# Performance work log

Measured on AMD Instinct MI355X. Metric: run time of the kernel, lower is better.

The kernel has to match this reference:

```python
import jax, jax.numpy as jnp
import numpy as np

HIDDEN = 2048
N_HEADS = 32
N_KV_HEADS = 8
HEAD_DIM = HIDDEN // N_HEADS  # 64
KV_DIM = N_KV_HEADS * HEAD_DIM  # 512


def setup_inputs() -> dict:
    key = jax.random.key(0)
    ks = jax.random.split(key, 9)
    s = 1.0 / np.sqrt(HIDDEN)
    x = jax.random.normal(ks[0], (2, 2048, HIDDEN), dtype=jnp.float32)
    wq = jax.random.uniform(ks[1], (HIDDEN, HIDDEN), jnp.float32, -s, s)
    bq = jax.random.uniform(ks[2], (HIDDEN,), jnp.float32, -s, s)
    wk = jax.random.uniform(ks[3], (KV_DIM, HIDDEN), jnp.float32, -s, s)
    bk = jax.random.uniform(ks[4], (KV_DIM,), jnp.float32, -s, s)
    wv = jax.random.uniform(ks[5], (KV_DIM, HIDDEN), jnp.float32, -s, s)
    bv = jax.random.uniform(ks[6], (KV_DIM,), jnp.float32, -s, s)
    wo = jax.random.uniform(ks[7], (HIDDEN, HIDDEN), jnp.float32, -s, s)
    bo = jax.random.uniform(ks[8], (HIDDEN,), jnp.float32, -s, s)
    return {"x": x, "wq": wq, "bq": bq, "wk": wk, "bk": bk,
            "wv": wv, "bv": bv, "wo": wo, "bo": bo}


def reference(x, wq, bq, wk, bk, wv, bv, wo, bo):
    B, S, _ = x.shape
    group = N_HEADS // N_KV_HEADS  # 4
    # projections (torch Linear: x @ W.T + b)
    q = (x @ wq.T + bq).reshape(B, S, N_HEADS, HEAD_DIM).transpose(0, 2, 1, 3)      # [B,H,S,D]
    k = (x @ wk.T + bk).reshape(B, S, N_KV_HEADS, HEAD_DIM).transpose(0, 2, 1, 3)   # [B,Hk,S,D]
    v = (x @ wv.T + bv).reshape(B, S, N_KV_HEADS, HEAD_DIM).transpose(0, 2, 1, 3)
    # repeat_interleave KV heads to match query heads
    k = jnp.repeat(k, group, axis=1)  # [B,H,S,D]
    v = jnp.repeat(v, group, axis=1)
    scale = 1.0 / np.sqrt(HEAD_DIM).astype(np.float32)
    attn = jnp.einsum('bhqd,bhkd->bhqk', q, k) * scale  # [B,H,S,S]
    score = jax.nn.softmax(attn, axis=-1)
    out = jnp.einsum('bhqk,bhkd->bhqd', score, v)       # [B,H,S,D]
    out = out.transpose(0, 2, 1, 3).reshape(B, S, HIDDEN)
    return out @ wo.T + bo
```

## Files before the change

### kernel.cpp

```cpp
#include <hip/hip_runtime.h>

typedef __attribute__((ext_vector_type(8))) short bf16x8;
typedef __attribute__((ext_vector_type(4))) float f32x4;
typedef __attribute__((ext_vector_type(16))) float f32x16;
typedef __attribute__((ext_vector_type(2))) float f32x2;

__device__ __forceinline__ short f2b(float f) {
  union { unsigned u; float f; } c;
  c.f = f;
  unsigned r = (c.u + 0x7FFFu + ((c.u >> 16) & 1u)) >> 16;
  return (short)r;
}

__device__ __forceinline__ int cvt_pk_bf16(float lo, float hi) {
  int r;
  asm("v_cvt_pk_bf16_f32 %0, %1, %2" : "=v"(r) : "v"(lo), "v"(hi));
  return r;
}

__device__ __forceinline__ void plswap(int& a, int& b) {
  asm volatile("v_permlane32_swap_b32 %0, %1" : "+v"(a), "+v"(b));
}

__device__ __forceinline__ f32x2 pk_add(f32x2 a, f32x2 b) {
  f32x2 d;
  asm("v_pk_add_f32 %0, %1, %2" : "=v"(d) : "v"(a), "v"(b));
  return d;
}

__device__ __forceinline__ unsigned permb(unsigned s0, unsigned s1, unsigned sel) {
  unsigned d;
  asm("v_perm_b32 %0, %1, %2, %3" : "=v"(d) : "v"(s0), "v"(s1), "s"(sel));
  return d;
}

__device__ __forceinline__ void async16(const void* g, void* l) {
  __builtin_amdgcn_global_load_lds(
      (const __attribute__((address_space(1))) unsigned*)g,
      (__attribute__((address_space(3))) unsigned*)l, 16, 0, 0);
}

__global__ __launch_bounds__(256)
void conv_all(const float* __restrict__ x,  const float* __restrict__ wq,
              const float* __restrict__ wk, const float* __restrict__ wv,
              const float* __restrict__ wo, short* __restrict__ dst) {
  const size_t M = 1048576;
  size_t i = ((size_t)blockIdx.x * 256 + threadIdx.x) * 4;
  const float* src; size_t off;
  if (i < 8 * M)       { src = x;  off = 0; }
  else if (i < 12 * M) { src = wq; off = 8 * M; }
  else if (i < 13 * M) { src = wk; off = 12 * M; }
  else if (i < 14 * M) { src = wv; off = 13 * M; }
  else                 { src = wo; off = 14 * M; }
  float4 v = *(const float4*)(src + (i - off));
  short4 o;
  o.x = f2b(v.x); o.y = f2b(v.y); o.z = f2b(v.z); o.w = f2b(v.w);
  *(short4*)(dst + i) = o;
}

template <bool F32OUT>
__global__ __launch_bounds__(256)
void gemm_bt_bias(const short* __restrict__ A, const short* __restrict__ Bw,
                  const float* __restrict__ bias, void* __restrict__ Cv,
                  int M, int N, int K) {
  __shared__ short lsA[128 * 32];
  __shared__ short lsB[128 * 32];
  const int tid  = threadIdx.x;
  const int wave = tid >> 6, lane = tid & 63;
  const int quad = lane >> 4, lrow = lane & 15;
  const int m0 = blockIdx.y * 128, n0 = blockIdx.x * 128;
  const int wm = (wave >> 1) * 64, wn = (wave & 1) * 64;

  f32x4 zero = {0.f, 0.f, 0.f, 0.f};
  f32x4 acc[4][4];
#pragma unroll
  for (int i = 0; i < 4; i++)
#pragma unroll
    for (int j = 0; j < 4; j++) acc[i][j] = zero;

  const int r0 = tid >> 2, c0 = (tid & 3) * 8;
  const short* Ab  = A  + (size_t)(m0 + r0) * K + c0;
  const short* Ab2 = A  + (size_t)(m0 + r0 + 64) * K + c0;
  const short* Bb  = Bw + (size_t)(n0 + r0) * K + c0;
  const short* Bb2 = Bw + (size_t)(n0 + r0 + 64) * K + c0;

  for (int k0 = 0; k0 < K; k0 += 32) {
    async16(Ab  + k0, lsA + tid * 8);
    async16(Ab2 + k0, lsA + (tid + 256) * 8);
    async16(Bb  + k0, lsB + tid * 8);
    async16(Bb2 + k0, lsB + (tid + 256) * 8);
    __syncthreads();

    bf16x8 af[4], bfr[4];
#pragma unroll
    for (int i = 0; i < 4; i++)
      af[i] = *(const bf16x8*)(lsA + (wm + i * 16 + lrow) * 32 + quad * 8);
#pragma unroll
    for (int j = 0; j < 4; j++)
      bfr[j] = *(const bf16x8*)(lsB + (wn + j * 16 + lrow) * 32 + quad * 8);
#pragma unroll
    for (int i = 0; i < 4; i++)
#pragma unroll
      for (int j = 0; j < 4; j++)
        acc[i][j] = __builtin_amdgcn_mfma_f32_16x16x32_bf16(af[i], bfr[j], acc[i][j], 0, 0, 0);
    __syncthreads();
  }

#pragma unroll
  for (int j = 0; j < 4; j++) {
    const int col = n0 + wn + j * 16 + lrow;
    const float bv = bias[col];
#pragma unroll
    for (int i = 0; i < 4; i++) {
      const int rowb = m0 + wm + i * 16 + quad * 4;
#pragma unroll
      for (int r = 0; r < 4; r++) {
        const float val = acc[i][j][r] + bv;
        if (F32OUT)
          ((float*)Cv)[(size_t)(rowb + r) * N + col] = val;
        else
          ((short*)Cv)[(size_t)(rowb + r) * N + col] = f2b(val);
      }
    }
  }
}

__global__ __launch_bounds__(256)
void gemm_qkv(const short* __restrict__ A, const short* __restrict__ Bw,
              const float* __restrict__ bq, const float* __restrict__ bk,
              const float* __restrict__ bv,
              short* __restrict__ Qo, short* __restrict__ Ko, short* __restrict__ Vo) {
  const int K = 2048;
  __shared__ short lsA[128 * 32];
  __shared__ short lsB[128 * 32];
  const int tid  = threadIdx.x;
  const int wave = tid >> 6, lane = tid & 63;
  const int quad = lane >> 4, lrow = lane & 15;
  const int m0 = blockIdx.y * 128, n0 = blockIdx.x * 128;
  const int wm = (wave >> 1) * 64, wn = (wave & 1) * 64;

  f32x4 zero = {0.f, 0.f, 0.f, 0.f};
  f32x4 acc[4][4];
#pragma unroll
  for (int i = 0; i < 4; i++)
#pragma unroll
    for (int j = 0; j < 4; j++) acc[i][j] = zero;

  const int r0 = tid >> 2, c0 = (tid & 3) * 8;
  const short* Ab  = A  + (size_t)(m0 + r0) * K + c0;
  const short* Ab2 = A  + (size_t)(m0 + r0 + 64) * K + c0;
  const short* Bb  = Bw + (size_t)(n0 + r0) * K + c0;
  const short* Bb2 = Bw + (size_t)(n0 + r0 + 64) * K + c0;

  for (int k0 = 0; k0 < K; k0 += 32) {
    async16(Ab  + k0, lsA + tid * 8);
    async16(Ab2 + k0, lsA + (tid + 256) * 8);
    async16(Bb  + k0, lsB + tid * 8);
    async16(Bb2 + k0, lsB + (tid + 256) * 8);
    __syncthreads();

    bf16x8 af[4], bfr[4];
#pragma unroll
    for (int i = 0; i < 4; i++)
      af[i] = *(const bf16x8*)(lsA + (wm + i * 16 + lrow) * 32 + quad * 8);
#pragma unroll
    for (int j = 0; j < 4; j++)
      bfr[j] = *(const bf16x8*)(lsB + (wn + j * 16 + lrow) * 32 + quad * 8);
#pragma unroll
    for (int i = 0; i < 4; i++)
#pragma unroll
      for (int j = 0; j < 4; j++)
        acc[i][j] = __builtin_amdgcn_mfma_f32_16x16x32_bf16(af[i], bfr[j], acc[i][j], 0, 0, 0);
    __syncthreads();
  }

  short* base; int stride, coff; const float* bias;
  if (n0 < 2048)      { base = Qo; stride = 2048; bias = bq; coff = 0; }
  else if (n0 < 2560) { base = Ko; stride = 512;  bias = bk; coff = 2048; }
  else                { base = Vo; stride = 512;  bias = bv; coff = 2560; }
  const float qs = (n0 < 2048) ? 0.18033688011112043f : 1.0f;

#pragma unroll
  for (int j = 0; j < 4; j++) {
    const int lc = n0 + wn + j * 16 + lrow - coff;
    const float bvv = bias[lc];
#pragma unroll
    for (int i = 0; i < 4; i++) {
      const int rowb = m0 + wm + i * 16 + quad * 4;
#pragma unroll
      for (int r = 0; r < 4; r++)
        base[(size_t)(rowb + r) * stride + lc] = f2b((acc[i][j][r] + bvv) * qs);
    }
  }
}

#define S_LEN 2048
#define HID   2048
#define KVD   512
#define ST    72

__global__ __launch_bounds__(256)
void gqa_flash(const short* __restrict__ Q, const short* __restrict__ Kb,
               const short* __restrict__ Vb, short* __restrict__ O) {
  __shared__ __align__(16) short lsK[64 * ST];
  __shared__ __align__(16) short lsVt[64 * ST];
  __shared__ float lsum[4][32];

  const int tid  = threadIdx.x;
  const int wave = tid >> 6, lane = tid & 63;
  const int l31  = lane & 31, hl = lane >> 5;

  const int d  = blockIdx.x + (blockIdx.y << 6);
  const int by = ((d & 7) << 1) | (d >> 9);
  const int qb = (d >> 3) & 63;
  const int b = by >> 3, kvh = by & 7;
  const int h = kvh * 4 + wave;
  const int q0 = qb * 32;

  const short* Qrow = Q + (size_t)(b * S_LEN + q0 + l31) * HID + h * 64 + hl * 8;
  bf16x8 qf[4];
#pragma unroll
  for (int f = 0; f < 4; f++) qf[f] = *(const bf16x8*)(Qrow + f * 16);

  f32x16 o0, o1;
#pragma unroll
  for (int i = 0; i < 16; i++) { o0[i] = 0.f; o1[i] = 0.f; }
  float lloc = 0.f;

  const short* Kp = Kb + (size_t)b * S_LEN * KVD + kvh * 64;
  const short* Vp = Vb + (size_t)b * S_LEN * KVD + kvh * 64;

  const int keyA = tid >> 3, chK = (tid & 7) * 8;
  const int kpV = tid & 31, dcV = (tid >> 5) * 8;

  bf16x8 kf0 = *(const bf16x8*)(Kp + (size_t)keyA * KVD + chK);
  bf16x8 kf1 = *(const bf16x8*)(Kp + (size_t)(keyA + 32) * KVD + chK);
  bf16x8 vf0 = *(const bf16x8*)(Vp + (size_t)(2 * kpV) * KVD + dcV);
  bf16x8 vf1 = *(const bf16x8*)(Vp + (size_t)(2 * kpV + 1) * KVD + dcV);

  for (int k0 = 0; k0 < S_LEN; k0 += 64) {
    *(bf16x8*)(lsK + keyA * ST + chK) = kf0;
    *(bf16x8*)(lsK + (keyA + 32) * ST + chK) = kf1;
    {
      const unsigned* u0 = (const unsigned*)&vf0;
      const unsigned* u1 = (const unsigned*)&vf1;
#pragma unroll
      for (int jw = 0; jw < 4; jw++) {
        unsigned lo = permb(u1[jw], u0[jw], 0x05040100u);
        unsigned hi = permb(u1[jw], u0[jw], 0x07060302u);
        *(unsigned*)(lsVt + (dcV + 2 * jw)     * ST + 2 * kpV) = lo;
        *(unsigned*)(lsVt + (dcV + 2 * jw + 1) * ST + 2 * kpV) = hi;
      }
    }
    __syncthreads();

    const int kn = (k0 + 64) & (S_LEN - 1);
    kf0 = *(const bf16x8*)(Kp + (size_t)(kn + keyA) * KVD + chK);
    kf1 = *(const bf16x8*)(Kp + (size_t)(kn + keyA + 32) * KVD + chK);
    vf0 = *(const bf16x8*)(Vp + (size_t)(kn + 2 * kpV) * KVD + dcV);
    vf1 = *(const bf16x8*)(Vp + (size_t)(kn + 2 * kpV + 1) * KVD + dcV);

    f32x16 s0, s1;
#pragma unroll
    for (int i = 0; i < 16; i++) { s0[i] = 0.f; s1[i] = 0.f; }
    __builtin_amdgcn_s_setprio(1);
#pragma unroll
    for (int f = 0; f < 4; f++) {
      bf16x8 ka = *(const bf16x8*)(lsK + l31 * ST + f * 16 + hl * 8);
      bf16x8 kb = *(const bf16x8*)(lsK + (32 + l31) * ST + f * 16 + hl * 8);
      s0 = __builtin_amdgcn_mfma_f32_32x32x16_bf16(ka, qf[f], s0, 0, 0, 0);
      s1 = __builtin_amdgcn_mfma_f32_32x32x16_bf16(kb, qf[f], s1, 0, 0, 0);
    }
    __builtin_amdgcn_s_setprio(0);

#pragma unroll
    for (int i = 0; i < 16; i++) {
      s0[i] = __builtin_amdgcn_exp2f(s0[i]);
      s1[i] = __builtin_amdgcn_exp2f(s1[i]);
    }
    {
      const f32x2* p0 = (const f32x2*)&s0;
      const f32x2* p1 = (const f32x2*)&s1;
      f32x2 t0 = pk_add(p0[0], p1[0]);
      f32x2 t1 = pk_add(p0[1], p1[1]);
      f32x2 t2 = pk_add(p0[2], p1[2]);
      f32x2 t3 = pk_add(p0[3], p1[3]);
      f32x2 t4 = pk_add(p0[4], p1[4]);
      f32x2 t5 = pk_add(p0[5], p1[5]);
      f32x2 t6 = pk_add(p0[6], p1[6]);
      f32x2 t7 = pk_add(p0[7], p1[7]);
      t0 = pk_add(t0, t4); t1 = pk_add(t1, t5);
      t2 = pk_add(t2, t6); t3 = pk_add(t3, t7);
      t0 = pk_add(t0, t2); t1 = pk_add(t1, t3);
      t0 = pk_add(t0, t1);
      lloc += t0.x + t0.y;
    }
    int P2[2][8];
#pragma unroll
    for (int qq = 0; qq < 8; qq++) {
      P2[0][qq] = cvt_pk_bf16(s0[2 * qq], s0[2 * qq + 1]);
      P2[1][qq] = cvt_pk_bf16(s1[2 * qq], s1[2 * qq + 1]);
    }

    __builtin_amdgcn_s_setprio(1);
#pragma unroll
    for (int t = 0; t < 4; t++) {
      const int j = t >> 1, b0 = (t & 1) * 4;
      int w0 = P2[j][b0 + 0], w2 = P2[j][b0 + 2];
      int w1 = P2[j][b0 + 1], w3 = P2[j][b0 + 3];
      plswap(w0, w2);
      plswap(w1, w3);
      union { unsigned u[4]; bf16x8 v; } pa;
      pa.u[0] = (unsigned)w0; pa.u[1] = (unsigned)w1;
      pa.u[2] = (unsigned)w2; pa.u[3] = (unsigned)w3;
      bf16x8 bv0 = *(const bf16x8*)(lsVt + l31 * ST + t * 16 + hl * 8);
      bf16x8 bv1 = *(const bf16x8*)(lsVt + (32 + l31) * ST + t * 16 + hl * 8);
      o0 = __builtin_amdgcn_mfma_f32_32x32x16_bf16(pa.v, bv0, o0, 0, 0, 0);
      o1 = __builtin_amdgcn_mfma_f32_32x32x16_bf16(pa.v, bv1, o1, 0, 0, 0);
    }
    __builtin_amdgcn_s_setprio(0);
    __syncthreads();
  }

  const float lfull = lloc + __shfl(lloc, lane ^ 32);
  if (lane < 32) lsum[wave][lane] = lfull;
#pragma unroll
  for (int r = 0; r < 16; r++) {
    const int qrow = (r & 3) + 8 * (r >> 2) + 4 * hl;
    const float rl = 1.0f / lsum[wave][qrow];
    short* op = O + (size_t)(b * S_LEN + q0 + qrow) * HID + h * 64 + l31;
    op[0]  = f2b(o0[r] * rl);
    op[32] = f2b(o1[r] * rl);
  }
}

extern "C" void kernel_launch(void* const* d_in, const int* in_sizes, int n_in,
                              void* d_out, int out_size, void* d_ws, size_t ws_size,
                              hipStream_t stream) {
  const float* x  = (const float*)d_in[0];
  const float* wq = (const float*)d_in[1];
  const float* bq = (const float*)d_in[2];
  const float* wk = (const float*)d_in[3];
  const float* bk = (const float*)d_in[4];
  const float* wv = (const float*)d_in[5];
  const float* bv = (const float*)d_in[6];
  const float* wo = (const float*)d_in[7];
  const float* bo = (const float*)d_in[8];
  float* out = (float*)d_out;

  short* xb  = (short*)d_ws;
  short* wqb = xb  + (size_t)4096 * 2048;
  short* wkb = wqb + (size_t)2048 * 2048;
  short* wvb = wkb + (size_t)512 * 2048;
  short* wob = wvb + (size_t)512 * 2048;
  short* Qb  = wob + (size_t)2048 * 2048;
  short* Kb  = Qb  + (size_t)4096 * 2048;
  short* Vb  = Kb  + (size_t)4096 * 512;
  short* AO  = Vb  + (size_t)4096 * 512;

  dim3 blk(256);
  conv_all<<<18 * 1048576 / 1024, blk, 0, stream>>>(x, wq, wk, wv, wo, xb);

  gemm_qkv<<<dim3(3072 / 128, 4096 / 128), blk, 0, stream>>>(xb, wqb, bq, bk, bv, Qb, Kb, Vb);
  gqa_flash<<<dim3(2048 / 32, 16), blk, 0, stream>>>(Qb, Kb, Vb, AO);
  gemm_bt_bias<true><<<dim3(2048 / 128, 4096 / 128), blk, 0, stream>>>(AO, wob, bo, out, 4096, 2048, 2048);
}
```

Before: 320.1 us.

## Widen GEMM k-tile with XOR-swizzled LDS and software-pipeline flash attention

Both GEMM kernels now stage 64-wide k-slices in LDS instead of 32-wide ones. Rows are stored with an XOR swizzle on 16-byte chunks, which halves the number of barrier pairs per K sweep and is meant to avoid LDS bank conflicts on the fragment reads. The attention kernel gets double-buffered K and V tiles: the P·V product of the previous tile is issued after the QK and softmax of the current tile, so MFMA work can overlap the exp/pack stage. The asm volatile on permlane swap is relaxed so the compiler can schedule it. The cost is twice the LDS per block and more live registers for the carried P fragments, which may lower occupancy.

```diff
diff --git a/kernel.cpp b/kernel.cpp
--- a/kernel.cpp
+++ b/kernel.cpp
@@ -19,7 +19,7 @@
 }
 
 __device__ __forceinline__ void plswap(int& a, int& b) {
-  asm volatile("v_permlane32_swap_b32 %0, %1" : "+v"(a), "+v"(b));
+  asm("v_permlane32_swap_b32 %0, %1" : "+v"(a), "+v"(b));
 }
 
 __device__ __forceinline__ f32x2 pk_add(f32x2 a, f32x2 b) {
@@ -63,8 +63,8 @@
 void gemm_bt_bias(const short* __restrict__ A, const short* __restrict__ Bw,
                   const float* __restrict__ bias, void* __restrict__ Cv,
                   int M, int N, int K) {
-  __shared__ short lsA[128 * 32];
-  __shared__ short lsB[128 * 32];
+  __shared__ short lsA[128 * 64];
+  __shared__ short lsB[128 * 64];
   const int tid  = threadIdx.x;
   const int wave = tid >> 6, lane = tid & 63;
   const int quad = lane >> 4, lrow = lane & 15;
@@ -78,31 +78,50 @@
 #pragma unroll
     for (int j = 0; j < 4; j++) acc[i][j] = zero;
 
-  const int r0 = tid >> 2, c0 = (tid & 3) * 8;
-  const short* Ab  = A  + (size_t)(m0 + r0) * K + c0;
-  const short* Ab2 = A  + (size_t)(m0 + r0 + 64) * K + c0;
-  const short* Bb  = Bw + (size_t)(n0 + r0) * K + c0;
-  const short* Bb2 = Bw + (size_t)(n0 + r0 + 64) * K + c0;
-
-  for (int k0 = 0; k0 < K; k0 += 32) {
-    async16(Ab  + k0, lsA + tid * 8);
-    async16(Ab2 + k0, lsA + (tid + 256) * 8);
-    async16(Bb  + k0, lsB + tid * 8);
-    async16(Bb2 + k0, lsB + (tid + 256) * 8);
-    __syncthreads();
-
-    bf16x8 af[4], bfr[4];
-#pragma unroll
-    for (int i = 0; i < 4; i++)
-      af[i] = *(const bf16x8*)(lsA + (wm + i * 16 + lrow) * 32 + quad * 8);
-#pragma unroll
-    for (int j = 0; j < 4; j++)
-      bfr[j] = *(const bf16x8*)(lsB + (wn + j * 16 + lrow) * 32 + quad * 8);
-#pragma unroll
-    for (int i = 0; i < 4; i++)
-#pragma unroll
-      for (int j = 0; j < 4; j++)
-        acc[i][j] = __builtin_amdgcn_mfma_f32_16x16x32_bf16(af[i], bfr[j], acc[i][j], 0, 0, 0);
+  const int R  = tid >> 3;
+  const int cs = tid & 7;
+  const int gc = (cs ^ (R & 7)) << 3;
+  const short* Arow[4]; const short* Brow[4];
+#pragma unroll
+  for (int b = 0; b < 4; b++) {
+    Arow[b] = A  + (size_t)(m0 + R + 32 * b) * K + gc;
+    Brow[b] = Bw + (size_t)(n0 + R + 32 * b) * K + gc;
+  }
+  const int ldst = R * 64 + cs * 8;
+
+  for (int k0 = 0; k0 < K; k0 += 64) {
+#pragma unroll
+    for (int b = 0; b < 4; b++) {
+      async16(Arow[b] + k0, lsA + ldst + b * 32 * 64);
+      async16(Brow[b] + k0, lsB + ldst + b * 32 * 64);
+    }
+    __syncthreads();
+
+    bf16x8 af[4][2], bfr[4][2];
+#pragma unroll
+    for (int i = 0; i < 4; i++) {
+      const int Rr = wm + i * 16 + lrow;
+#pragma unroll
+      for (int kk = 0; kk < 2; kk++)
+        af[i][kk] = *(const bf16x8*)(lsA + Rr * 64 +
+                                     (((kk * 4 + quad) ^ (Rr & 7)) << 3));
+    }
+#pragma unroll
+    for (int j = 0; j < 4; j++) {
+      const int Sr = wn + j * 16 + lrow;
+#pragma unroll
+      for (int kk = 0; kk < 2; kk++)
+        bfr[j][kk] = *(const bf16x8*)(lsB + Sr * 64 +
+                                      (((kk * 4 + quad) ^ (Sr & 7)) << 3));
+    }
+#pragma unroll
+    for (int kk = 0; kk < 2; kk++)
+#pragma unroll
+      for (int i = 0; i < 4; i++)
+#pragma unroll
+        for (int j = 0; j < 4; j++)
+          acc[i][j] = __builtin_amdgcn_mfma_f32_16x16x32_bf16(
+              af[i][kk], bfr[j][kk], acc[i][j], 0, 0, 0);
     __syncthreads();
   }
 
@@ -131,8 +150,8 @@
               const float* __restrict__ bv,
               short* __restrict__ Qo, short* __restrict__ Ko, short* __restrict__ Vo) {
   const int K = 2048;
-  __shared__ short lsA[128 * 32];
-  __shared__ short lsB[128 * 32];
+  __shared__ short lsA[128 * 64];
+  __shared__ short lsB[128 * 64];
   const int tid  = threadIdx.x;
   const int wave = tid >> 6, lane = tid & 63;
   const int quad = lane >> 4, lrow = lane & 15;
@@ -146,31 +165,50 @@
 #pragma unroll
     for (int j = 0; j < 4; j++) acc[i][j] = zero;
 
-  const int r0 = tid >> 2, c0 = (tid & 3) * 8;
-  const short* Ab  = A  + (size_t)(m0 + r0) * K + c0;
-  const short* Ab2 = A  + (size_t)(m0 + r0 + 64) * K + c0;
-  const short* Bb  = Bw + (size_t)(n0 + r0) * K + c0;
-  const short* Bb2 = Bw + (size_t)(n0 + r0 + 64) * K + c0;
-
-  for (int k0 = 0; k0 < K; k0 += 32) {
-    async16(Ab  + k0, lsA + tid * 8);
-    async16(Ab2 + k0, lsA + (tid + 256) * 8);
-    async16(Bb  + k0, lsB + tid * 8);
-    async16(Bb2 + k0, lsB + (tid + 256) * 8);
-    __syncthreads();
-
-    bf16x8 af[4], bfr[4];
-#pragma unroll
-    for (int i = 0; i < 4; i++)
-      af[i] = *(const bf16x8*)(lsA + (wm + i * 16 + lrow) * 32 + quad * 8);
-#pragma unroll
-    for (int j = 0; j < 4; j++)
-      bfr[j] = *(const bf16x8*)(lsB + (wn + j * 16 + lrow) * 32 + quad * 8);
-#pragma unroll
-    for (int i = 0; i < 4; i++)
-#pragma unroll
-      for (int j = 0; j < 4; j++)
-        acc[i][j] = __builtin_amdgcn_mfma_f32_16x16x32_bf16(af[i], bfr[j], acc[i][j], 0, 0, 0);
+  const int R  = tid >> 3;
+  const int cs = tid & 7;
+  const int gc = (cs ^ (R & 7)) << 3;
+  const short* Arow[4]; const short* Brow[4];
+#pragma unroll
+  for (int b = 0; b < 4; b++) {
+    Arow[b] = A  + (size_t)(m0 + R + 32 * b) * K + gc;
+    Brow[b] = Bw + (size_t)(n0 + R + 32 * b) * K + gc;
+  }
+  const int ldst = R * 64 + cs * 8;
+
+  for (int k0 = 0; k0 < K; k0 += 64) {
+#pragma unroll
+    for (int b = 0; b < 4; b++) {
+      async16(Arow[b] + k0, lsA + ldst + b * 32 * 64);
+      async16(Brow[b] + k0, lsB + ldst + b * 32 * 64);
+    }
+    __syncthreads();
+
+    bf16x8 af[4][2], bfr[4][2];
+#pragma unroll
+    for (int i = 0; i < 4; i++) {
+      const int Rr = wm + i * 16 + lrow;
+#pragma unroll
+      for (int kk = 0; kk < 2; kk++)
+        af[i][kk] = *(const bf16x8*)(lsA + Rr * 64 +
+                                     (((kk * 4 + quad) ^ (Rr & 7)) << 3));
+    }
+#pragma unroll
+    for (int j = 0; j < 4; j++) {
+      const int Sr = wn + j * 16 + lrow;
+#pragma unroll
+      for (int kk = 0; kk < 2; kk++)
+        bfr[j][kk] = *(const bf16x8*)(lsB + Sr * 64 +
+                                      (((kk * 4 + quad) ^ (Sr & 7)) << 3));
+    }
+#pragma unroll
+    for (int kk = 0; kk < 2; kk++)
+#pragma unroll
+      for (int i = 0; i < 4; i++)
+#pragma unroll
+        for (int j = 0; j < 4; j++)
+          acc[i][j] = __builtin_amdgcn_mfma_f32_16x16x32_bf16(
+              af[i][kk], bfr[j][kk], acc[i][j], 0, 0, 0);
     __syncthreads();
   }
 
@@ -202,8 +240,8 @@
 __global__ __launch_bounds__(256)
 void gqa_flash(const short* __restrict__ Q, const short* __restrict__ Kb,
                const short* __restrict__ Vb, short* __restrict__ O) {
-  __shared__ __align__(16) short lsK[64 * ST];
-  __shared__ __align__(16) short lsVt[64 * ST];
+  __shared__ __align__(16) short lsK[2][64 * ST];
+  __shared__ __align__(16) short lsVt[2][64 * ST];
   __shared__ float lsum[4][32];
 
   const int tid  = threadIdx.x;
@@ -233,46 +271,45 @@
   const int keyA = tid >> 3, chK = (tid & 7) * 8;
   const int kpV = tid & 31, dcV = (tid >> 5) * 8;
 
-  bf16x8 kf0 = *(const bf16x8*)(Kp + (size_t)keyA * KVD + chK);
-  bf16x8 kf1 = *(const bf16x8*)(Kp + (size_t)(keyA + 32) * KVD + chK);
-  bf16x8 vf0 = *(const bf16x8*)(Vp + (size_t)(2 * kpV) * KVD + dcV);
-  bf16x8 vf1 = *(const bf16x8*)(Vp + (size_t)(2 * kpV + 1) * KVD + dcV);
-
-  for (int k0 = 0; k0 < S_LEN; k0 += 64) {
-    *(bf16x8*)(lsK + keyA * ST + chK) = kf0;
-    *(bf16x8*)(lsK + (keyA + 32) * ST + chK) = kf1;
-    {
-      const unsigned* u0 = (const unsigned*)&vf0;
-      const unsigned* u1 = (const unsigned*)&vf1;
-#pragma unroll
-      for (int jw = 0; jw < 4; jw++) {
-        unsigned lo = permb(u1[jw], u0[jw], 0x05040100u);
-        unsigned hi = permb(u1[jw], u0[jw], 0x07060302u);
-        *(unsigned*)(lsVt + (dcV + 2 * jw)     * ST + 2 * kpV) = lo;
-        *(unsigned*)(lsVt + (dcV + 2 * jw + 1) * ST + 2 * kpV) = hi;
-      }
-    }
-    __syncthreads();
-
-    const int kn = (k0 + 64) & (S_LEN - 1);
+  bf16x8 kf0, kf1, vf0, vf1;
+  auto prefetch = [&](int kt) {
+    const int kn = (kt * 64) & (S_LEN - 1);
     kf0 = *(const bf16x8*)(Kp + (size_t)(kn + keyA) * KVD + chK);
     kf1 = *(const bf16x8*)(Kp + (size_t)(kn + keyA + 32) * KVD + chK);
     vf0 = *(const bf16x8*)(Vp + (size_t)(kn + 2 * kpV) * KVD + dcV);
     vf1 = *(const bf16x8*)(Vp + (size_t)(kn + 2 * kpV + 1) * KVD + dcV);
-
-    f32x16 s0, s1;
+  };
+  auto commit = [&](int bs) {
+    *(bf16x8*)(lsK[bs] + keyA * ST + chK) = kf0;
+    *(bf16x8*)(lsK[bs] + (keyA + 32) * ST + chK) = kf1;
+    const unsigned* u0 = (const unsigned*)&vf0;
+    const unsigned* u1 = (const unsigned*)&vf1;
+#pragma unroll
+    for (int jw = 0; jw < 4; jw++) {
+      unsigned lo = permb(u1[jw], u0[jw], 0x05040100u);
+      unsigned hi = permb(u1[jw], u0[jw], 0x07060302u);
+      *(unsigned*)(lsVt[bs] + (dcV + 2 * jw)     * ST + 2 * kpV) = lo;
+      *(unsigned*)(lsVt[bs] + (dcV + 2 * jw + 1) * ST + 2 * kpV) = hi;
+    }
+  };
+
+  f32x16 s0, s1;
+  auto qk = [&](int bs) {
 #pragma unroll
     for (int i = 0; i < 16; i++) { s0[i] = 0.f; s1[i] = 0.f; }
     __builtin_amdgcn_s_setprio(1);
 #pragma unroll
     for (int f = 0; f < 4; f++) {
-      bf16x8 ka = *(const bf16x8*)(lsK + l31 * ST + f * 16 + hl * 8);
-      bf16x8 kb = *(const bf16x8*)(lsK + (32 + l31) * ST + f * 16 + hl * 8);
+      bf16x8 ka = *(const bf16x8*)(lsK[bs] + l31 * ST + f * 16 + hl * 8);
+      bf16x8 kb = *(const bf16x8*)(lsK[bs] + (32 + l31) * ST + f * 16 + hl * 8);
       s0 = __builtin_amdgcn_mfma_f32_32x32x16_bf16(ka, qf[f], s0, 0, 0, 0);
       s1 = __builtin_amdgcn_mfma_f32_32x32x16_bf16(kb, qf[f], s1, 0, 0, 0);
     }
     __builtin_amdgcn_s_setprio(0);
-
+  };
+
+  bf16x8 pav0, pav1, pav2, pav3;
+  auto softmax_pack = [&](bf16x8& n0v, bf16x8& n1v, bf16x8& n2v, bf16x8& n3v) {
 #pragma unroll
     for (int i = 0; i < 16; i++) {
       s0[i] = __builtin_amdgcn_exp2f(s0[i]);
@@ -301,8 +338,7 @@
       P2[0][qq] = cvt_pk_bf16(s0[2 * qq], s0[2 * qq + 1]);
       P2[1][qq] = cvt_pk_bf16(s1[2 * qq], s1[2 * qq + 1]);
     }
-
-    __builtin_amdgcn_s_setprio(1);
+    bf16x8* outs[4] = {&n0v, &n1v, &n2v, &n3v};
 #pragma unroll
     for (int t = 0; t < 4; t++) {
       const int j = t >> 1, b0 = (t & 1) * 4;
@@ -313,14 +349,40 @@
       union { unsigned u[4]; bf16x8 v; } pa;
       pa.u[0] = (unsigned)w0; pa.u[1] = (unsigned)w1;
       pa.u[2] = (unsigned)w2; pa.u[3] = (unsigned)w3;
-      bf16x8 bv0 = *(const bf16x8*)(lsVt + l31 * ST + t * 16 + hl * 8);
-      bf16x8 bv1 = *(const bf16x8*)(lsVt + (32 + l31) * ST + t * 16 + hl * 8);
-      o0 = __builtin_amdgcn_mfma_f32_32x32x16_bf16(pa.v, bv0, o0, 0, 0, 0);
-      o1 = __builtin_amdgcn_mfma_f32_32x32x16_bf16(pa.v, bv1, o1, 0, 0, 0);
-    }
-    __builtin_amdgcn_s_setprio(0);
-    __syncthreads();
-  }
+      *outs[t] = pa.v;
+    }
+  };
+  auto pv = [&](int bp) {
+    bf16x8 pv_[4] = {pav0, pav1, pav2, pav3};
+#pragma unroll
+    for (int t = 0; t < 4; t++) {
+      bf16x8 bv0 = *(const bf16x8*)(lsVt[bp] + l31 * ST + t * 16 + hl * 8);
+      bf16x8 bv1 = *(const bf16x8*)(lsVt[bp] + (32 + l31) * ST + t * 16 + hl * 8);
+      o0 = __builtin_amdgcn_mfma_f32_32x32x16_bf16(pv_[t], bv0, o0, 0, 0, 0);
+      o1 = __builtin_amdgcn_mfma_f32_32x32x16_bf16(pv_[t], bv1, o1, 0, 0, 0);
+    }
+  };
+
+  prefetch(0);
+  commit(0);
+  __syncthreads();
+  prefetch(1);
+  qk(0);
+  softmax_pack(pav0, pav1, pav2, pav3);
+
+  for (int t = 1; t < S_LEN / 64; t++) {
+    const int bs = t & 1, bp = bs ^ 1;
+    commit(bs);
+    __syncthreads();
+    prefetch(t + 1);
+    qk(bs);
+    bf16x8 n0v, n1v, n2v, n3v;
+    softmax_pack(n0v, n1v, n2v, n3v);
+    pv(bp);
+    pav0 = n0v; pav1 = n1v; pav2 = n2v; pav3 = n3v;
+    __syncthreads();
+  }
+  pv(1);
 
   const float lfull = lloc + __shfl(lloc, lane ^ 32);
   if (lane < 32) lsum[wave][lane] = lfull;
```

Result: slower. 332.6 us (+3.9%).

## Switch projection GEMMs to 32x32 MFMA with K=64 swizzled LDS tiles and XCD remap

Applied to the files above, without the earlier changes.

Both projection GEMM kernels now use 32x32x16 bf16 MFMA instead of 16x16x32, stage 64-wide K slices per iteration, and XOR-swizzle the LDS layout to avoid bank conflicts on fragment reads. Workgroup IDs are remapped so consecutive tiles land on the same XCD, which should improve L2 reuse. This halves the number of barrier pairs per GEMM and improves MFMA-to-load ratio, at the cost of doubled LDS footprint. The permlane swap asm also loses its volatile qualifier so the compiler can schedule it more freely.

```diff
diff --git a/kernel.cpp b/kernel.cpp
--- a/kernel.cpp
+++ b/kernel.cpp
@@ -19,7 +19,7 @@
 }
 
 __device__ __forceinline__ void plswap(int& a, int& b) {
-  asm volatile("v_permlane32_swap_b32 %0, %1" : "+v"(a), "+v"(b));
+  asm("v_permlane32_swap_b32 %0, %1" : "+v"(a), "+v"(b));
 }
 
 __device__ __forceinline__ f32x2 pk_add(f32x2 a, f32x2 b) {
@@ -63,63 +63,90 @@
 void gemm_bt_bias(const short* __restrict__ A, const short* __restrict__ Bw,
                   const float* __restrict__ bias, void* __restrict__ Cv,
                   int M, int N, int K) {
-  __shared__ short lsA[128 * 32];
-  __shared__ short lsB[128 * 32];
+  __shared__ short lsA[128 * 64];
+  __shared__ short lsB[128 * 64];
   const int tid  = threadIdx.x;
   const int wave = tid >> 6, lane = tid & 63;
-  const int quad = lane >> 4, lrow = lane & 15;
-  const int m0 = blockIdx.y * 128, n0 = blockIdx.x * 128;
+  const int l31  = lane & 31, hl = lane >> 5;
+  const int GX  = gridDim.x;
+  const int nwg = GX * gridDim.y;
+  const int dd  = blockIdx.x + blockIdx.y * GX;
+  const int logical = (dd & 7) * (nwg >> 3) + (dd >> 3);
+  const int m0 = (logical / GX) * 128, n0 = (logical % GX) * 128;
   const int wm = (wave >> 1) * 64, wn = (wave & 1) * 64;
 
-  f32x4 zero = {0.f, 0.f, 0.f, 0.f};
-  f32x4 acc[4][4];
-#pragma unroll
-  for (int i = 0; i < 4; i++)
-#pragma unroll
-    for (int j = 0; j < 4; j++) acc[i][j] = zero;
-
-  const int r0 = tid >> 2, c0 = (tid & 3) * 8;
-  const short* Ab  = A  + (size_t)(m0 + r0) * K + c0;
-  const short* Ab2 = A  + (size_t)(m0 + r0 + 64) * K + c0;
-  const short* Bb  = Bw + (size_t)(n0 + r0) * K + c0;
-  const short* Bb2 = Bw + (size_t)(n0 + r0 + 64) * K + c0;
-
-  for (int k0 = 0; k0 < K; k0 += 32) {
-    async16(Ab  + k0, lsA + tid * 8);
-    async16(Ab2 + k0, lsA + (tid + 256) * 8);
-    async16(Bb  + k0, lsB + tid * 8);
-    async16(Bb2 + k0, lsB + (tid + 256) * 8);
-    __syncthreads();
-
-    bf16x8 af[4], bfr[4];
-#pragma unroll
-    for (int i = 0; i < 4; i++)
-      af[i] = *(const bf16x8*)(lsA + (wm + i * 16 + lrow) * 32 + quad * 8);
-#pragma unroll
-    for (int j = 0; j < 4; j++)
-      bfr[j] = *(const bf16x8*)(lsB + (wn + j * 16 + lrow) * 32 + quad * 8);
-#pragma unroll
-    for (int i = 0; i < 4; i++)
-#pragma unroll
-      for (int j = 0; j < 4; j++)
-        acc[i][j] = __builtin_amdgcn_mfma_f32_16x16x32_bf16(af[i], bfr[j], acc[i][j], 0, 0, 0);
-    __syncthreads();
-  }
-
-#pragma unroll
-  for (int j = 0; j < 4; j++) {
-    const int col = n0 + wn + j * 16 + lrow;
-    const float bv = bias[col];
-#pragma unroll
-    for (int i = 0; i < 4; i++) {
-      const int rowb = m0 + wm + i * 16 + quad * 4;
-#pragma unroll
-      for (int r = 0; r < 4; r++) {
-        const float val = acc[i][j][r] + bv;
+  f32x16 acc[2][2];
+#pragma unroll
+  for (int i = 0; i < 2; i++)
+#pragma unroll
+    for (int j = 0; j < 2; j++)
+#pragma unroll
+      for (int r = 0; r < 16; r++) acc[i][j][r] = 0.f;
+
+  const int R  = tid >> 3;
+  const int cs = tid & 7;
+  const int gc = (cs ^ (R & 7)) << 3;
+  const short* Arow[4]; const short* Brow[4];
+#pragma unroll
+  for (int b = 0; b < 4; b++) {
+    Arow[b] = A  + (size_t)(m0 + R + 32 * b) * K + gc;
+    Brow[b] = Bw + (size_t)(n0 + R + 32 * b) * K + gc;
+  }
+  const int ldst = R * 64 + cs * 8;
+
+  for (int k0 = 0; k0 < K; k0 += 64) {
+#pragma unroll
+    for (int b = 0; b < 4; b++) {
+      async16(Arow[b] + k0, lsA + ldst + b * 32 * 64);
+      async16(Brow[b] + k0, lsB + ldst + b * 32 * 64);
+    }
+    __syncthreads();
+
+    bf16x8 af[2][4], bfr[2][4];
+#pragma unroll
+    for (int i = 0; i < 2; i++) {
+      const int Rr = wm + i * 32 + l31;
+#pragma unroll
+      for (int kq = 0; kq < 4; kq++) {
+        const int c = kq * 2 + hl;
+        af[i][kq] = *(const bf16x8*)(lsA + Rr * 64 + ((c ^ (Rr & 7)) << 3));
+      }
+    }
+#pragma unroll
+    for (int j = 0; j < 2; j++) {
+      const int Sr = wn + j * 32 + l31;
+#pragma unroll
+      for (int kq = 0; kq < 4; kq++) {
+        const int c = kq * 2 + hl;
+        bfr[j][kq] = *(const bf16x8*)(lsB + Sr * 64 + ((c ^ (Sr & 7)) << 3));
+      }
+    }
+#pragma unroll
+    for (int kq = 0; kq < 4; kq++)
+#pragma unroll
+      for (int i = 0; i < 2; i++)
+#pragma unroll
+        for (int j = 0; j < 2; j++)
+          acc[i][j] = __builtin_amdgcn_mfma_f32_32x32x16_bf16(
+              af[i][kq], bfr[j][kq], acc[i][j], 0, 0, 0);
+    __syncthreads();
+  }
+
+#pragma unroll
+  for (int j = 0; j < 2; j++) {
+    const int col = n0 + wn + j * 32 + l31;
+    const float bb = bias[col];
+#pragma unroll
+    for (int i = 0; i < 2; i++) {
+      const int rowb = m0 + wm + i * 32;
+#pragma unroll
+      for (int r = 0; r < 16; r++) {
+        const int row = rowb + (r & 3) + 8 * (r >> 2) + 4 * hl;
+        const float val = acc[i][j][r] + bb;
         if (F32OUT)
-          ((float*)Cv)[(size_t)(rowb + r) * N + col] = val;
+          ((float*)Cv)[(size_t)row * N + col] = val;
         else
-          ((short*)Cv)[(size_t)(rowb + r) * N + col] = f2b(val);
+          ((short*)Cv)[(size_t)row * N + col] = f2b(val);
       }
     }
   }
@@ -131,46 +158,72 @@
               const float* __restrict__ bv,
               short* __restrict__ Qo, short* __restrict__ Ko, short* __restrict__ Vo) {
   const int K = 2048;
-  __shared__ short lsA[128 * 32];
-  __shared__ short lsB[128 * 32];
+  __shared__ short lsA[128 * 64];
+  __shared__ short lsB[128 * 64];
   const int tid  = threadIdx.x;
   const int wave = tid >> 6, lane = tid & 63;
-  const int quad = lane >> 4, lrow = lane & 15;
-  const int m0 = blockIdx.y * 128, n0 = blockIdx.x * 128;
+  const int l31  = lane & 31, hl = lane >> 5;
+  const int GX  = gridDim.x;
+  const int nwg = GX * gridDim.y;
+  const int dd  = blockIdx.x + blockIdx.y * GX;
+  const int logical = (dd & 7) * (nwg >> 3) + (dd >> 3);
+  const int m0 = (logical / GX) * 128, n0 = (logical % GX) * 128;
   const int wm = (wave >> 1) * 64, wn = (wave & 1) * 64;
 
-  f32x4 zero = {0.f, 0.f, 0.f, 0.f};
-  f32x4 acc[4][4];
-#pragma unroll
-  for (int i = 0; i < 4; i++)
-#pragma unroll
-    for (int j = 0; j < 4; j++) acc[i][j] = zero;
-
-  const int r0 = tid >> 2, c0 = (tid & 3) * 8;
-  const short* Ab  = A  + (size_t)(m0 + r0) * K + c0;
-  const short* Ab2 = A  + (size_t)(m0 + r0 + 64) * K + c0;
-  const short* Bb  = Bw + (size_t)(n0 + r0) * K + c0;
-  const short* Bb2 = Bw + (size_t)(n0 + r0 + 64) * K + c0;
-
-  for (int k0 = 0; k0 < K; k0 += 32) {
-    async16(Ab  + k0, lsA + tid * 8);
-    async16(Ab2 + k0, lsA + (tid + 256) * 8);
-    async16(Bb  + k0, lsB + tid * 8);
-    async16(Bb2 + k0, lsB + (tid + 256) * 8);
-    __syncthreads();
-
-    bf16x8 af[4], bfr[4];
-#pragma unroll
-    for (int i = 0; i < 4; i++)
-      af[i] = *(const bf16x8*)(lsA + (wm + i * 16 + lrow) * 32 + quad * 8);
-#pragma unroll
-    for (int j = 0; j < 4; j++)
-      bfr[j] = *(const bf16x8*)(lsB + (wn + j * 16 + lrow) * 32 + quad * 8);
-#pragma unroll
-    for (int i = 0; i < 4; i++)
-#pragma unroll
-      for (int j = 0; j < 4; j++)
-        acc[i][j] = __builtin_amdgcn_mfma_f32_16x16x32_bf16(af[i], bfr[j], acc[i][j], 0, 0, 0);
+  f32x16 acc[2][2];
+#pragma unroll
+  for (int i = 0; i < 2; i++)
+#pragma unroll
+    for (int j = 0; j < 2; j++)
+#pragma unroll
+      for (int r = 0; r < 16; r++) acc[i][j][r] = 0.f;
+
+  const int R  = tid >> 3;
+  const int cs = tid & 7;
+  const int gc = (cs ^ (R & 7)) << 3;
+  const short* Arow[4]; const short* Brow[4];
+#pragma unroll
+  for (int b = 0; b < 4; b++) {
+    Arow[b] = A  + (size_t)(m0 + R + 32 * b) * K + gc;
+    Brow[b] = Bw + (size_t)(n0 + R + 32 * b) * K + gc;
+  }
+  const int ldst = R * 64 + cs * 8;
+
+  for (int k0 = 0; k0 < K; k0 += 64) {
+#pragma unroll
+    for (int b = 0; b < 4; b++) {
+      async16(Arow[b] + k0, lsA + ldst + b * 32 * 64);
+      async16(Brow[b] + k0, lsB + ldst + b * 32 * 64);
+    }
+    __syncthreads();
+
+    bf16x8 af[2][4], bfr[2][4];
+#pragma unroll
+    for (int i = 0; i < 2; i++) {
+      const int Rr = wm + i * 32 + l31;
+#pragma unroll
+      for (int kq = 0; kq < 4; kq++) {
+        const int c = kq * 2 + hl;
+        af[i][kq] = *(const bf16x8*)(lsA + Rr * 64 + ((c ^ (Rr & 7)) << 3));
+      }
+    }
+#pragma unroll
+    for (int j = 0; j < 2; j++) {
+      const int Sr = wn + j * 32 + l31;
+#pragma unroll
+      for (int kq = 0; kq < 4; kq++) {
+        const int c = kq * 2 + hl;
+        bfr[j][kq] = *(const bf16x8*)(lsB + Sr * 64 + ((c ^ (Sr & 7)) << 3));
+      }
+    }
+#pragma unroll
+    for (int kq = 0; kq < 4; kq++)
+#pragma unroll
+      for (int i = 0; i < 2; i++)
+#pragma unroll
+        for (int j = 0; j < 2; j++)
+          acc[i][j] = __builtin_amdgcn_mfma_f32_32x32x16_bf16(
+              af[i][kq], bfr[j][kq], acc[i][j], 0, 0, 0);
     __syncthreads();
   }
 
@@ -181,15 +234,17 @@
   const float qs = (n0 < 2048) ? 0.18033688011112043f : 1.0f;
 
 #pragma unroll
-  for (int j = 0; j < 4; j++) {
-    const int lc = n0 + wn + j * 16 + lrow - coff;
-    const float bvv = bias[lc];
-#pragma unroll
-    for (int i = 0; i < 4; i++) {
-      const int rowb = m0 + wm + i * 16 + quad * 4;
-#pragma unroll
-      for (int r = 0; r < 4; r++)
-        base[(size_t)(rowb + r) * stride + lc] = f2b((acc[i][j][r] + bvv) * qs);
+  for (int j = 0; j < 2; j++) {
+    const int lc = n0 + wn + j * 32 + l31 - coff;
+    const float bb = bias[lc];
+#pragma unroll
+    for (int i = 0; i < 2; i++) {
+      const int rowb = m0 + wm + i * 32;
+#pragma unroll
+      for (int r = 0; r < 16; r++) {
+        const int row = rowb + (r & 3) + 8 * (r >> 2) + 4 * hl;
+        base[(size_t)row * stride + lc] = f2b((acc[i][j][r] + bb) * qs);
+      }
     }
   }
 }
```

Result: no change. 315.6 us (-1.4%).
